# Optimization experiments

Hardware: AMD Instinct MI355X
Metric: run time of the kernel (lower is better)

Reference implementation:

```python
import jax, jax.numpy as jnp
import numpy as np

B, P, L = 8, 196, 80
DIM1, DIM2, ATT = 2048, 300, 1024


def setup_inputs() -> dict:
    key = jax.random.key(0)
    ks = jax.random.split(key, 8)
    s1 = 1.0 / np.sqrt(DIM1)
    s2 = 1.0 / np.sqrt(DIM2)
    sa = 1.0 / np.sqrt(ATT)
    return {
        "x1": jax.random.normal(ks[0], (B, P, DIM1), jnp.float32),
        "x2": jax.random.normal(ks[1], (B, L, DIM2), jnp.float32),
        "W1": jax.random.uniform(ks[2], (ATT, DIM1), jnp.float32, -s1, s1),
        "W2": jax.random.uniform(ks[3], (ATT, DIM2), jnp.float32, -s2, s2),
        "Wh": jax.random.uniform(ks[4], (ATT, ATT), jnp.float32, -sa, sa),
        "bh": jax.random.uniform(ks[5], (ATT,), jnp.float32, -sa, sa),
        "wt": jax.random.uniform(ks[6], (ATT,), jnp.float32, -sa, sa),
        "bt": jax.random.uniform(ks[7], (), jnp.float32, -sa, sa),
    }


def reference(x1, x2, W1, W2, Wh, bh, wt, bt):
    # project: p1 (B,P,A), p2 (B,L,A)
    p1 = jnp.einsum("bpd,ad->bpa", x1, W1)
    p2 = jnp.einsum("bld,ad->bla", x2, W2)
    # broadcast bilinear + tanh: (B,L,P,A)
    h = jnp.tanh(p1[:, None, :, :] * p2[:, :, None, :])
    # hidden linear then target linear (rank-1 on last dim)
    t = jnp.einsum("blpa,ca->blpc", h, Wh) + bh
    alpha = jnp.einsum("blpc,c->blp", t, wt) + bt  # (B,L,P)
    return alpha
```

## Files before the change

### kernel.cpp

```cpp
#include <hip/hip_runtime.h>
#include <hip/hip_bf16.h>

static constexpr int kB   = 8;
static constexpr int kP   = 196;
static constexpr int kL   = 80;
static constexpr int kD1  = 2048;
static constexpr int kD2  = 300;
static constexpr int kD2p = 320;
static constexpr int kATT = 1024;
static constexpr int kM   = kB * kP;
static constexpr int kR2  = kB * kL;
static constexpr int kASplit = 8;
static constexpr int kAChunk = kATT / kASplit;
static constexpr int kLPer   = 5;

static constexpr float kTanhScale = 2.8853900817779268f;

__device__ __forceinline__ unsigned short f2bf(float x) {
    union { float f; unsigned int u; } c; c.f = x;
    unsigned int r = c.u + 0x7fffu + ((c.u >> 16) & 1u);
    return (unsigned short)(r >> 16);
}

typedef __attribute__((ext_vector_type(8))) short  bf16x8;
typedef __attribute__((ext_vector_type(4))) float  f32x4;

__device__ __forceinline__ void load_lds16(const void* g, void* l) {
    __builtin_amdgcn_global_load_lds(
        (const __attribute__((address_space(1))) void*)g,
        (__attribute__((address_space(3))) void*)l, 16, 0, 0);
}

__global__ __launch_bounds__(256) void cast_all_kernel(
        const float* __restrict__ x1, unsigned short* __restrict__ x1b,
        const float* __restrict__ W1, unsigned short* __restrict__ W1b,
        const float* __restrict__ x2, unsigned short* __restrict__ x2b,
        const float* __restrict__ W2, unsigned short* __restrict__ W2b) {
    const int n4a = kM * kD1 / 4;
    const int n4b = kATT * kD1 / 4;
    const int n1  = kR2 * kD2p;
    const int n2  = kATT * kD2p;
    int i = blockIdx.x * 256 + threadIdx.x;
    if (i < n4a) {
        float4 f = ((const float4*)x1)[i];
        ushort4 o = { f2bf(f.x), f2bf(f.y), f2bf(f.z), f2bf(f.w) };
        ((ushort4*)x1b)[i] = o;
    } else if ((i -= n4a) < n4b) {
        float4 f = ((const float4*)W1)[i];
        ushort4 o = { f2bf(f.x), f2bf(f.y), f2bf(f.z), f2bf(f.w) };
        ((ushort4*)W1b)[i] = o;
    } else if ((i -= n4b) < n1) {
        int r = i / kD2p, c = i - r * kD2p;
        x2b[i] = (c < kD2) ? f2bf(x2[(size_t)r * kD2 + c]) : (unsigned short)0;
    } else if ((i -= n1) < n2) {
        int r = i / kD2p, c = i - r * kD2p;
        W2b[i] = (c < kD2) ? f2bf(W2[(size_t)r * kD2 + c]) : (unsigned short)0;
    }
}

__global__ __launch_bounds__(256) void vbeta_kernel(
        const float* __restrict__ Wh, const float* __restrict__ wt,
        const float* __restrict__ bh, const float* __restrict__ bt,
        float* __restrict__ v, float* __restrict__ beta) {
    const int a  = blockIdx.x * 256 + threadIdx.x;
    const int c0 = blockIdx.y * 64;
    float acc = 0.0f;
    #pragma unroll 8
    for (int c = c0; c < c0 + 64; ++c)
        acc = fmaf(wt[c], Wh[(size_t)c * kATT + a], acc);
    atomicAdd(&v[a], acc);

    if (blockIdx.x == 0 && threadIdx.x < 64) {
        int c = c0 + threadIdx.x;
        float pb = wt[c] * bh[c];
        #pragma unroll
        for (int off = 32; off > 0; off >>= 1)
            pb += __shfl_down(pb, off, 64);
        if (threadIdx.x == 0) {
            if (blockIdx.y == 0) pb += bt[0];
            atomicAdd(beta, pb);
        }
    }
}

static constexpr int kP2Blocks = (kR2 / 64) * (kATT / 64);
static constexpr int kP1Blocks = ((kM + 63) / 64) * (kATT / 64);

__global__ __launch_bounds__(256) void gemm_all_kernel(
        const unsigned short* __restrict__ x2b, const unsigned short* __restrict__ W2b,
        float* __restrict__ p2w,
        const unsigned short* __restrict__ x1b, const unsigned short* __restrict__ W1b,
        float* __restrict__ p1w) {
    __shared__ unsigned short As[64 * 64];
    __shared__ unsigned short Bs[64 * 64];

    const unsigned short *Ab, *Bb;
    float* Co; int M, K, mx, nx; float scale;
    {
        int bid = blockIdx.x;
        if (bid < kP2Blocks) {
            Ab = x2b; Bb = W2b; Co = p2w; M = kR2; K = kD2p; scale = 1.0f;
            mx = bid % (kR2 / 64); nx = bid / (kR2 / 64);
        } else {
            int l = bid - kP2Blocks;
            Ab = x1b; Bb = W1b; Co = p1w; M = kM; K = kD1; scale = kTanhScale;
            mx = l % ((kM + 63) / 64); nx = l / ((kM + 63) / 64);
        }
    }
    const int m0   = mx * 64;
    const int n0   = nx * 64;
    const int tid  = threadIdx.x;
    const int lane = tid & 63;
    const int wv   = tid >> 6;
    const int mh   = (wv >> 1) * 32;
    const int nh   = (wv & 1) * 32;

    const int row0 = tid >> 3,        ko0 = (tid & 7) * 8;
    const int row1 = (tid + 256) >> 3, ko1 = (tid & 7) * 8;
    const int ar0 = min(m0 + row0, M - 1), ar1 = min(m0 + row1, M - 1);
    const int br0 = n0 + row0,            br1 = n0 + row1;

    f32x4 acc[2][2] = {};
    for (int k0 = 0; k0 < K; k0 += 64) {
        load_lds16(Ab + (size_t)ar0 * K + k0 + ko0, (char*)As + tid * 16);
        load_lds16(Ab + (size_t)ar1 * K + k0 + ko1, (char*)As + (tid + 256) * 16);
        load_lds16(Bb + (size_t)br0 * K + k0 + ko0, (char*)Bs + tid * 16);
        load_lds16(Bb + (size_t)br1 * K + k0 + ko1, (char*)Bs + (tid + 256) * 16);
        __syncthreads();

        #pragma unroll
        for (int kk = 0; kk < 2; ++kk) {
            bf16x8 af[2], bf[2];
            #pragma unroll
            for (int i = 0; i < 2; ++i) {
                int r = mh + i * 16 + (lane & 15);
                af[i] = *(const bf16x8*)((const char*)As + r * 128 + kk * 64 + (lane >> 4) * 16);
            }
            #pragma unroll
            for (int j = 0; j < 2; ++j) {
                int r = nh + j * 16 + (lane & 15);
                bf[j] = *(const bf16x8*)((const char*)Bs + r * 128 + kk * 64 + (lane >> 4) * 16);
            }
            #pragma unroll
            for (int i = 0; i < 2; ++i)
                #pragma unroll
                for (int j = 0; j < 2; ++j)
                    acc[i][j] = __builtin_amdgcn_mfma_f32_16x16x32_bf16(
                                    af[i], bf[j], acc[i][j], 0, 0, 0);
        }
        __syncthreads();
    }

    #pragma unroll
    for (int i = 0; i < 2; ++i)
        #pragma unroll
        for (int j = 0; j < 2; ++j)
            #pragma unroll
            for (int r = 0; r < 4; ++r) {
                int m = m0 + mh + i * 16 + (lane >> 4) * 4 + r;
                int n = n0 + nh + j * 16 + (lane & 15);
                if (m < M) Co[(size_t)m * kATT + n] = scale * acc[i][j][r];
            }
}

__global__ __launch_bounds__(256) void alpha_kernel(
        const float* __restrict__ p1, const float* __restrict__ p2,
        const float* __restrict__ v, const float* __restrict__ beta,
        float* __restrict__ out) {
    __shared__ float vs[kAChunk];
    __shared__ float sred;
    const int b     = blockIdx.y;
    const int as    = blockIdx.z;
    const int aBase = as * kAChunk;
    const int p0    = blockIdx.x * 16;
    const int tid   = threadIdx.x;
    const int tp    = tid & 15;
    const int lg    = tid >> 4;

    if (tid < kAChunk) vs[tid] = v[aBase + tid];
    __syncthreads();
    if (tid < 64) {
        float s = vs[tid] + vs[tid + 64];
        #pragma unroll
        for (int off = 32; off > 0; off >>= 1)
            s += __shfl_down(s, off, 64);
        if (tid == 0) sred = s;
    }
    __syncthreads();
    const float sumV = sred;

    const int p   = p0 + tp;
    const int gr1 = b * kP + min(p, kP - 1);
    const float* pu = p1 + (size_t)gr1 * kATT + aBase;
    const float* pw = p2 + ((size_t)(b * kL + lg * kLPer)) * kATT + aBase;

    float acc[kLPer] = {};
    #pragma unroll 2
    for (int a4 = 0; a4 < kAChunk / 4; ++a4) {
        float4 u  = *(const float4*)(pu + a4 * 4);
        float4 vv = *(const float4*)&vs[a4 * 4];
        #pragma unroll
        for (int j = 0; j < kLPer; ++j) {
            float4 w = *(const float4*)(pw + (size_t)j * kATT + a4 * 4);
            acc[j] = fmaf(vv.x, __builtin_amdgcn_rcpf(__builtin_amdgcn_exp2f(u.x * w.x) + 1.0f), acc[j]);
            acc[j] = fmaf(vv.y, __builtin_amdgcn_rcpf(__builtin_amdgcn_exp2f(u.y * w.y) + 1.0f), acc[j]);
            acc[j] = fmaf(vv.z, __builtin_amdgcn_rcpf(__builtin_amdgcn_exp2f(u.z * w.z) + 1.0f), acc[j]);
            acc[j] = fmaf(vv.w, __builtin_amdgcn_rcpf(__builtin_amdgcn_exp2f(u.w * w.w) + 1.0f), acc[j]);
        }
    }
    if (p < kP) {
        const float bb = (as == 0) ? beta[0] : 0.0f;
        #pragma unroll
        for (int j = 0; j < kLPer; ++j) {
            float res = sumV - 2.0f * acc[j] + bb;
            atomicAdd(&out[((size_t)b * kL + lg * kLPer + j) * kP + p], res);
        }
    }
}

extern "C" void kernel_launch(void* const* d_in, const int* in_sizes, int n_in,
                              void* d_out, int out_size, void* d_ws, size_t ws_size,
                              hipStream_t stream) {
    const float* x1 = (const float*)d_in[0];
    const float* x2 = (const float*)d_in[1];
    const float* W1 = (const float*)d_in[2];
    const float* W2 = (const float*)d_in[3];
    const float* Wh = (const float*)d_in[4];
    const float* bh = (const float*)d_in[5];
    const float* wt = (const float*)d_in[6];
    const float* bt = (const float*)d_in[7];
    float* out = (float*)d_out;

    float* ws   = (float*)d_ws;
    float* v    = ws;
    float* beta = ws + 1024;
    float* p2w  = ws + 1088;
    float* p1w  = p2w + (size_t)kR2 * kATT;
    unsigned short* x1b = (unsigned short*)(p1w + (size_t)kM * kATT);
    unsigned short* W1b = x1b + (size_t)kM * kD1;
    unsigned short* x2b = W1b + (size_t)kATT * kD1;
    unsigned short* W2b = x2b + (size_t)kR2 * kD2p;

    hipMemsetAsync(ws, 0, 1088 * sizeof(float), stream);
    hipMemsetAsync(out, 0, (size_t)out_size * sizeof(float), stream);

    {
        int n = kM * kD1 / 4 + kATT * kD1 / 4 + kR2 * kD2p + kATT * kD2p;
        cast_all_kernel<<<dim3((n + 255) / 256), 256, 0, stream>>>(
            x1, x1b, W1, W1b, x2, x2b, W2, W2b);
    }
    vbeta_kernel<<<dim3(4, 16), 256, 0, stream>>>(Wh, wt, bh, bt, v, beta);
    gemm_all_kernel<<<dim3(kP2Blocks + kP1Blocks), 256, 0, stream>>>(
        x2b, W2b, p2w, x1b, W1b, p1w);
    alpha_kernel<<<dim3((kP + 15) / 16, kB, kASplit), 256, 0, stream>>>(
        p1w, p2w, v, beta, out);
}
```

Measured before the change: 161.1 us.

## Merge prep kernels, double alpha A-split, replace output atomics with partial-sum reduce

Folds the v/beta reduction into the bf16 cast kernel as extra blocks, saving a launch. It doubles the split of the attention dimension in the alpha kernel to 16 chunks for more parallelism. Each chunk now writes partial results to a workspace buffer, and a new reduce kernel sums them and adds beta, replacing atomicAdd on the output and the output memset. The cost is an extra kernel launch, more workspace traffic, and redundant sumV code in the shared reduction.

```diff
diff --git a/kernel.cpp b/kernel.cpp
--- a/kernel.cpp
+++ b/kernel.cpp
@@ -10,7 +10,8 @@
 static constexpr int kATT = 1024;
 static constexpr int kM   = kB * kP;
 static constexpr int kR2  = kB * kL;
-static constexpr int kASplit = 8;
+static constexpr int kOut = kB * kL * kP;
+static constexpr int kASplit = 16;
 static constexpr int kAChunk = kATT / kASplit;
 static constexpr int kLPer   = 5;
 
@@ -31,55 +32,59 @@
         (__attribute__((address_space(3))) void*)l, 16, 0, 0);
 }
 
-__global__ __launch_bounds__(256) void cast_all_kernel(
+static constexpr int kN4a = kM * kD1 / 4;
+static constexpr int kN4b = kATT * kD1 / 4;
+static constexpr int kN1  = kR2 * kD2p;
+static constexpr int kN2  = kATT * kD2p;
+static constexpr int kCastBlocks =
+    (kN4a + kN4b + kN1 + kN2 + 255) / 256;
+
+__global__ __launch_bounds__(256) void prep_kernel(
         const float* __restrict__ x1, unsigned short* __restrict__ x1b,
         const float* __restrict__ W1, unsigned short* __restrict__ W1b,
         const float* __restrict__ x2, unsigned short* __restrict__ x2b,
-        const float* __restrict__ W2, unsigned short* __restrict__ W2b) {
-    const int n4a = kM * kD1 / 4;
-    const int n4b = kATT * kD1 / 4;
-    const int n1  = kR2 * kD2p;
-    const int n2  = kATT * kD2p;
+        const float* __restrict__ W2, unsigned short* __restrict__ W2b,
+        const float* __restrict__ Wh, const float* __restrict__ wt,
+        const float* __restrict__ bh, const float* __restrict__ bt,
+        float* __restrict__ v, float* __restrict__ beta) {
+    if (blockIdx.x >= kCastBlocks) {
+        int bid = blockIdx.x - kCastBlocks;
+        int ax  = bid & 3;
+        int c0  = (bid >> 2) * 64;
+        int a   = ax * 256 + threadIdx.x;
+        float acc = 0.0f;
+        #pragma unroll 8
+        for (int c = c0; c < c0 + 64; ++c)
+            acc = fmaf(wt[c], Wh[(size_t)c * kATT + a], acc);
+        atomicAdd(&v[a], acc);
+        if (ax == 0 && threadIdx.x < 64) {
+            int c = c0 + threadIdx.x;
+            float pb = wt[c] * bh[c];
+            #pragma unroll
+            for (int off = 32; off > 0; off >>= 1)
+                pb += __shfl_down(pb, off, 64);
+            if (threadIdx.x == 0) {
+                if (c0 == 0) pb += bt[0];
+                atomicAdd(beta, pb);
+            }
+        }
+        return;
+    }
     int i = blockIdx.x * 256 + threadIdx.x;
-    if (i < n4a) {
+    if (i < kN4a) {
         float4 f = ((const float4*)x1)[i];
         ushort4 o = { f2bf(f.x), f2bf(f.y), f2bf(f.z), f2bf(f.w) };
         ((ushort4*)x1b)[i] = o;
-    } else if ((i -= n4a) < n4b) {
+    } else if ((i -= kN4a) < kN4b) {
         float4 f = ((const float4*)W1)[i];
         ushort4 o = { f2bf(f.x), f2bf(f.y), f2bf(f.z), f2bf(f.w) };
         ((ushort4*)W1b)[i] = o;
-    } else if ((i -= n4b) < n1) {
+    } else if ((i -= kN4b) < kN1) {
         int r = i / kD2p, c = i - r * kD2p;
         x2b[i] = (c < kD2) ? f2bf(x2[(size_t)r * kD2 + c]) : (unsigned short)0;
-    } else if ((i -= n1) < n2) {
+    } else if ((i -= kN1) < kN2) {
         int r = i / kD2p, c = i - r * kD2p;
         W2b[i] = (c < kD2) ? f2bf(W2[(size_t)r * kD2 + c]) : (unsigned short)0;
-    }
-}
-
-__global__ __launch_bounds__(256) void vbeta_kernel(
-        const float* __restrict__ Wh, const float* __restrict__ wt,
-        const float* __restrict__ bh, const float* __restrict__ bt,
-        float* __restrict__ v, float* __restrict__ beta) {
-    const int a  = blockIdx.x * 256 + threadIdx.x;
-    const int c0 = blockIdx.y * 64;
-    float acc = 0.0f;
-    #pragma unroll 8
-    for (int c = c0; c < c0 + 64; ++c)
-        acc = fmaf(wt[c], Wh[(size_t)c * kATT + a], acc);
-    atomicAdd(&v[a], acc);
-
-    if (blockIdx.x == 0 && threadIdx.x < 64) {
-        int c = c0 + threadIdx.x;
-        float pb = wt[c] * bh[c];
-        #pragma unroll
-        for (int off = 32; off > 0; off >>= 1)
-            pb += __shfl_down(pb, off, 64);
-        if (threadIdx.x == 0) {
-            if (blockIdx.y == 0) pb += bt[0];
-            atomicAdd(beta, pb);
-        }
     }
 }
 
@@ -115,10 +120,10 @@
     const int mh   = (wv >> 1) * 32;
     const int nh   = (wv & 1) * 32;
 
-    const int row0 = tid >> 3,        ko0 = (tid & 7) * 8;
+    const int row0 = tid >> 3,         ko0 = (tid & 7) * 8;
     const int row1 = (tid + 256) >> 3, ko1 = (tid & 7) * 8;
     const int ar0 = min(m0 + row0, M - 1), ar1 = min(m0 + row1, M - 1);
-    const int br0 = n0 + row0,            br1 = n0 + row1;
+    const int br0 = n0 + row0,             br1 = n0 + row1;
 
     f32x4 acc[2][2] = {};
     for (int k0 = 0; k0 < K; k0 += 64) {
@@ -165,8 +170,7 @@
 
 __global__ __launch_bounds__(256) void alpha_kernel(
         const float* __restrict__ p1, const float* __restrict__ p2,
-        const float* __restrict__ v, const float* __restrict__ beta,
-        float* __restrict__ out) {
+        const float* __restrict__ v, float* __restrict__ part) {
     __shared__ float vs[kAChunk];
     __shared__ float sred;
     const int b     = blockIdx.y;
@@ -180,7 +184,9 @@
     if (tid < kAChunk) vs[tid] = v[aBase + tid];
     __syncthreads();
     if (tid < 64) {
-        float s = vs[tid] + vs[tid + 64];
+        float s = vs[tid & (kAChunk - 1)] * ((tid < kAChunk) ? 1.0f : 0.0f);
+        s = vs[tid < kAChunk ? tid : 0];
+        if (tid >= kAChunk) s = 0.0f;
         #pragma unroll
         for (int off = 32; off > 0; off >>= 1)
             s += __shfl_down(s, off, 64);
@@ -209,12 +215,23 @@
         }
     }
     if (p < kP) {
-        const float bb = (as == 0) ? beta[0] : 0.0f;
-        #pragma unroll
-        for (int j = 0; j < kLPer; ++j) {
-            float res = sumV - 2.0f * acc[j] + bb;
-            atomicAdd(&out[((size_t)b * kL + lg * kLPer + j) * kP + p], res);
-        }
+        float* po = part + (size_t)as * kOut + ((size_t)b * kL + lg * kLPer) * kP + p;
+        #pragma unroll
+        for (int j = 0; j < kLPer; ++j)
+            po[(size_t)j * kP] = sumV - 2.0f * acc[j];
+    }
+}
+
+__global__ __launch_bounds__(256) void reduce_kernel(
+        const float* __restrict__ part, const float* __restrict__ beta,
+        float* __restrict__ out) {
+    int i = blockIdx.x * 256 + threadIdx.x;
+    if (i < kOut) {
+        float s = beta[0];
+        #pragma unroll
+        for (int r = 0; r < kASplit; ++r)
+            s += part[(size_t)r * kOut + i];
+        out[i] = s;
     }
 }
 
@@ -240,18 +257,15 @@
     unsigned short* W1b = x1b + (size_t)kM * kD1;
     unsigned short* x2b = W1b + (size_t)kATT * kD1;
     unsigned short* W2b = x2b + (size_t)kR2 * kD2p;
+    float* part = (float*)(W2b + (size_t)kATT * kD2p);
 
     hipMemsetAsync(ws, 0, 1088 * sizeof(float), stream);
-    hipMemsetAsync(out, 0, (size_t)out_size * sizeof(float), stream);
-
-    {
-        int n = kM * kD1 / 4 + kATT * kD1 / 4 + kR2 * kD2p + kATT * kD2p;
-        cast_all_kernel<<<dim3((n + 255) / 256), 256, 0, stream>>>(
-            x1, x1b, W1, W1b, x2, x2b, W2, W2b);
-    }
-    vbeta_kernel<<<dim3(4, 16), 256, 0, stream>>>(Wh, wt, bh, bt, v, beta);
+
+    prep_kernel<<<dim3(kCastBlocks + 64), 256, 0, stream>>>(
+        x1, x1b, W1, W1b, x2, x2b, W2, W2b, Wh, wt, bh, bt, v, beta);
     gemm_all_kernel<<<dim3(kP2Blocks + kP1Blocks), 256, 0, stream>>>(
         x2b, W2b, p2w, x1b, W1b, p1w);
     alpha_kernel<<<dim3((kP + 15) / 16, kB, kASplit), 256, 0, stream>>>(
-        p1w, p2w, v, beta, out);
-}
+        p1w, p2w, v, part);
+    reduce_kernel<<<dim3((kOut + 255) / 256), 256, 0, stream>>>(part, beta, out);
+}
```

Result: faster. 154.1 us (-4.4%).
